# Kernel optimization log

Hardware: AMD Instinct MI355X
Metric: run time of the kernel (lower is better)

Reference implementation:

```python
import jax, jax.numpy as jnp
import numpy as np

DIM = 256
HEADS = 8
H = 56
W = 56
WS = 7          # window size
SHIFT = 3       # cyclic shift
MLP_HIDDEN = 4 * DIM
HEAD_DIM = DIM // HEADS
SCALE = HEAD_DIM ** -0.5
N = WS * WS     # tokens per window
EPS = 1e-5


def _rel_pos_index():
    coords = np.stack(np.meshgrid(np.arange(WS), np.arange(WS), indexing='ij'))  # [2,ws,ws]
    cf = coords.reshape(2, -1)                       # [2, N]
    rel = cf[:, :, None] - cf[:, None, :]            # [2, N, N]
    rel = rel.transpose(1, 2, 0).copy()              # [N, N, 2]
    rel[:, :, 0] += WS - 1
    rel[:, :, 1] += WS - 1
    rel[:, :, 1] *= 2 * WS - 1
    return rel.sum(-1)                               # [N, N]

REL_IDX = jnp.asarray(_rel_pos_index())


def _attn_mask():
    # shifted-window attention mask, computed once (static)
    img = np.zeros((H, W))
    cnt = 0
    slices = (slice(0, -WS), slice(-WS, -SHIFT), slice(-SHIFT, None))
    for hs in slices:
        for ws in slices:
            img[hs, ws] = cnt
            cnt += 1
    mw = img.reshape(H // WS, WS, W // WS, WS).transpose(0, 2, 1, 3).reshape(-1, N)  # [nW, N]
    am = mw[:, None, :] - mw[:, :, None]
    return jnp.asarray(np.where(am != 0, -100.0, 0.0).astype(np.float32))  # [nW, N, N]

ATTN_MASK = _attn_mask()


def _layernorm(y, g, b):
    mu = y.mean(-1, keepdims=True)
    var = ((y - mu) ** 2).mean(-1, keepdims=True)
    return (y - mu) * jax.lax.rsqrt(var + EPS) * g + b


def setup_inputs() -> dict:
    key = jax.random.key(0)
    ks = jax.random.split(key, 10)
    B = 32
    x = jax.random.normal(ks[0], (B, H * W, DIM), dtype=jnp.float32)
    qkv_w = jax.random.normal(ks[1], (DIM, 3 * DIM), dtype=jnp.float32) * 0.02
    qkv_b = jnp.zeros((3 * DIM,), dtype=jnp.float32)
    proj_w = jax.random.normal(ks[2], (DIM, DIM), dtype=jnp.float32) * 0.02
    proj_b = jnp.zeros((DIM,), dtype=jnp.float32)
    bias_table = jax.random.normal(ks[3], ((2 * WS - 1) * (2 * WS - 1), HEADS), dtype=jnp.float32) * 0.02
    norm1_g = jnp.ones((DIM,), dtype=jnp.float32)
    norm1_b = jnp.zeros((DIM,), dtype=jnp.float32)
    norm2_g = jnp.ones((DIM,), dtype=jnp.float32)
    norm2_b = jnp.zeros((DIM,), dtype=jnp.float32)
    mlp_w1 = jax.random.normal(ks[4], (DIM, MLP_HIDDEN), dtype=jnp.float32) * 0.02
    mlp_b1 = jnp.zeros((MLP_HIDDEN,), dtype=jnp.float32)
    mlp_w2 = jax.random.normal(ks[5], (MLP_HIDDEN, DIM), dtype=jnp.float32) * 0.02
    mlp_b2 = jnp.zeros((DIM,), dtype=jnp.float32)
    return dict(x=x, norm1_g=norm1_g, norm1_b=norm1_b, qkv_w=qkv_w, qkv_b=qkv_b,
                proj_w=proj_w, proj_b=proj_b, bias_table=bias_table,
                norm2_g=norm2_g, norm2_b=norm2_b,
                mlp_w1=mlp_w1, mlp_b1=mlp_b1, mlp_w2=mlp_w2, mlp_b2=mlp_b2)


def reference(x, norm1_g, norm1_b, qkv_w, qkv_b, proj_w, proj_b, bias_table,
              norm2_g, norm2_b, mlp_w1, mlp_b1, mlp_w2, mlp_b2):
    B, M, C = x.shape
    shortcut = x
    y = _layernorm(x, norm1_g, norm1_b).reshape(B, H, W, C)
    # cyclic shift
    y = jnp.roll(y, (-SHIFT, -SHIFT), axis=(1, 2))
    # window partition: [B,H,W,C] -> [B*nW, N, C]
    win = y.reshape(B, H // WS, WS, W // WS, WS, C).transpose(0, 1, 3, 2, 4, 5).reshape(-1, N, C)
    Bw = win.shape[0]
    qkv = (win @ qkv_w + qkv_b).reshape(Bw, N, 3, HEADS, HEAD_DIM).transpose(2, 0, 3, 1, 4)
    q, k, v = qkv[0], qkv[1], qkv[2]               # each [Bw, heads, N, hd]
    attn = jnp.einsum('bhnd,bhmd->bhnm', q, k) * SCALE
    bias = bias_table[REL_IDX].transpose(2, 0, 1)  # [heads, N, N]
    attn = attn + bias[None]
    nW = ATTN_MASK.shape[0]
    attn = attn.reshape(B, nW, HEADS, N, N) + ATTN_MASK[None, :, None]
    attn = jax.nn.softmax(attn.reshape(Bw, HEADS, N, N), axis=-1)
    out = jnp.einsum('bhnm,bhmd->bhnd', attn, v).transpose(0, 2, 1, 3).reshape(Bw, N, C)
    out = out @ proj_w + proj_b
    # window reverse and un-shift
    out = out.reshape(B, H // WS, W // WS, WS, WS, C).transpose(0, 1, 3, 2, 4, 5).reshape(B, H, W, C)
    out = jnp.roll(out, (SHIFT, SHIFT), axis=(1, 2)).reshape(B, M, C)
    x = shortcut + out
    h = _layernorm(x, norm2_g, norm2_b)
    h = jax.nn.gelu(h @ mlp_w1 + mlp_b1) @ mlp_w2 + mlp_b2
    return x + h
```

## Files before the change

kernel.cpp:

```cpp
#include <hip/hip_runtime.h>
#include <hip/hip_bf16.h>
#include <math.h>

typedef __bf16 bf16_t;
typedef __attribute__((ext_vector_type(8))) __bf16 bf16x8;
typedef __attribute__((ext_vector_type(4))) __bf16 bf16x4;
typedef __attribute__((ext_vector_type(4))) float f32x4;

#define T_TOK 100352
#define DIMC 256
#define HEADS 8
#define HD 32
#define NTOK 49
#define SHIFT3 3
#define HH 56
#define SCALE_QK 0.17677669529663687f

__device__ __forceinline__ int xrow_of(int rr) {
    int wi = rr / 49; int t = rr - wi * 49;
    int b = wi >> 6; int w64 = wi & 63;
    int wh = w64 >> 3, ww = w64 & 7;
    int i = t / 7, j = t - i * 7;
    int hy = wh * 7 + i, wy = ww * 7 + j;
    int hx = hy + SHIFT3; if (hx >= HH) hx -= HH;
    int wx = wy + SHIFT3; if (wx >= HH) wx -= HH;
    return b * (HH * HH) + hx * HH + wx;
}

__global__ __launch_bounds__(256) void transpose_all(const float* __restrict__ qkv_w,
                                                     const float* __restrict__ proj_w,
                                                     const float* __restrict__ w1,
                                                     const float* __restrict__ w2,
                                                     bf16_t* __restrict__ wt_qkv,
                                                     bf16_t* __restrict__ wt_proj,
                                                     bf16_t* __restrict__ wt_mlp1,
                                                     bf16_t* __restrict__ wt_mlp2) {
    int t = blockIdx.x * 256 + threadIdx.x;
    const float* W; bf16_t* WT; int K, Nc;
    if (t < 196608)      { W = qkv_w;  WT = wt_qkv;  K = 256;  Nc = 768;  }
    else if (t < 262144) { W = proj_w; WT = wt_proj; K = 256;  Nc = 256;  t -= 196608; }
    else if (t < 524288) { W = w1;     WT = wt_mlp1; K = 256;  Nc = 1024; t -= 262144; }
    else                 { W = w2;     WT = wt_mlp2; K = 1024; Nc = 256;  t -= 524288; }
    int k = t / Nc, c = t - k * Nc;
    WT[(size_t)c * K + k] = (bf16_t)W[t];
}

template <int MAP>
__global__ __launch_bounds__(256) void ln_kernel(const float* __restrict__ x,
                                                 const float* __restrict__ g,
                                                 const float* __restrict__ bsh,
                                                 bf16_t* __restrict__ out) {
    int wv = threadIdx.x >> 6, l = threadIdx.x & 63;
    int r = blockIdx.x * 4 + wv;
    int xr = MAP ? xrow_of(r) : r;
    float4 v = ((const float4*)(x + (size_t)xr * DIMC))[l];
    float s = v.x + v.y + v.z + v.w;
    float sq = v.x * v.x + v.y * v.y + v.z * v.z + v.w * v.w;
    #pragma unroll
    for (int off = 32; off; off >>= 1) {
        s += __shfl_down(s, off);
        sq += __shfl_down(sq, off);
    }
    s = __shfl(s, 0); sq = __shfl(sq, 0);
    float mean = s * (1.f / 256.f);
    float var = sq * (1.f / 256.f) - mean * mean;
    float rstd = rsqrtf(var + 1e-5f);
    float4 gv = ((const float4*)g)[l];
    float4 bv = ((const float4*)bsh)[l];
    bf16x4 o;
    o[0] = (bf16_t)((v.x - mean) * rstd * gv.x + bv.x);
    o[1] = (bf16_t)((v.y - mean) * rstd * gv.y + bv.y);
    o[2] = (bf16_t)((v.z - mean) * rstd * gv.z + bv.z);
    o[3] = (bf16_t)((v.w - mean) * rstd * gv.w + bv.w);
    *(bf16x4*)(out + (size_t)r * DIMC + l * 4) = o;
}

template <int EPI, int KT>
__global__ __launch_bounds__(512, 4) void gemm_a(const bf16_t* __restrict__ A,
                                                 const bf16_t* __restrict__ BT,
                                                 const float* __restrict__ bias,
                                                 int Nc,
                                                 bf16_t* __restrict__ outb,
                                                 float* __restrict__ outf,
                                                 const float* __restrict__ resid) {
    constexpr int NS = KT / 32;
    __shared__ __align__(16) char S[3][24576];
    int tid = threadIdx.x;
    int wv = tid >> 6, l = tid & 63;
    int wr = wv >> 2, wc = wv & 3;
    int nTilesN = Nc >> 8;
    int qn = gridDim.x >> 3;
    int lb = (blockIdx.x & 7) * qn + (blockIdx.x >> 3);
    int bm = lb / nTilesN, bn = lb - bm * nTilesN;
    size_t row0 = (size_t)bm * 128;
    int col0 = bn * 256;

    const char* Abase = (const char*)(A + row0 * KT);
    const char* Bbase = (const char*)(BT + (size_t)col0 * KT);
    const size_t ldb = (size_t)KT * 2;

    auto STAGE = [&](int b, int kk) {
        {
            int ci = tid;
            int sup = ci >> 3, slot = ci & 7;
            int us = slot ^ (sup & 7);
            int row = 2 * sup + (us >> 2), ch = us & 3;
            __builtin_amdgcn_global_load_lds(
                (const __attribute__((address_space(1))) void*)(Abase + (size_t)row * ldb + (size_t)kk * 2 + ch * 16),
                (__attribute__((address_space(3))) void*)(S[b] + ci * 16), 16, 0, 0);
        }
        #pragma unroll
        for (int it = 0; it < 2; ++it) {
            int ci = tid + it * 512;
            int sup = ci >> 3, slot = ci & 7;
            int us = slot ^ (sup & 7);
            int row = 2 * sup + (us >> 2), ch = us & 3;
            __builtin_amdgcn_global_load_lds(
                (const __attribute__((address_space(1))) void*)(Bbase + (size_t)row * ldb + (size_t)kk * 2 + ch * 16),
                (__attribute__((address_space(3))) void*)(S[b] + 8192 + ci * 16), 16, 0, 0);
        }
    };

    f32x4 acc[4][4] = {};
    const int lr = l & 15, g4 = l >> 4;

    STAGE(0, 0);
    STAGE(1, 32);

    #pragma unroll
    for (int s = 0; s < NS; ++s) {
        if (s + 1 < NS) { asm volatile("s_waitcnt vmcnt(3)" ::: "memory"); }
        else            { asm volatile("s_waitcnt vmcnt(0)" ::: "memory"); }
        __builtin_amdgcn_s_barrier();
        __builtin_amdgcn_sched_barrier(0);
        int buf = s % 3;
        if (s + 2 < NS) STAGE((s + 2) % 3, (s + 2) * 32);
        const char* Sb = S[buf];
        bf16x8 a[4], b[4];
        #pragma unroll
        for (int mt = 0; mt < 4; ++mt) {
            int r = wr * 64 + mt * 16 + lr;
            int sup = r >> 1;
            int us = ((r & 1) << 2) | g4;
            a[mt] = *(const bf16x8*)(Sb + sup * 128 + ((us ^ (sup & 7)) * 16));
        }
        #pragma unroll
        for (int nt = 0; nt < 4; ++nt) {
            int rc = wc * 64 + nt * 16 + lr;
            int sup = rc >> 1;
            int us = ((rc & 1) << 2) | g4;
            b[nt] = *(const bf16x8*)(Sb + 8192 + sup * 128 + ((us ^ (sup & 7)) * 16));
        }
        __builtin_amdgcn_s_setprio(1);
        #pragma unroll
        for (int mt = 0; mt < 4; ++mt)
            #pragma unroll
            for (int nt = 0; nt < 4; ++nt)
                acc[mt][nt] = __builtin_amdgcn_mfma_f32_16x16x32_bf16(a[mt], b[nt], acc[mt][nt], 0, 0, 0);
        __builtin_amdgcn_s_setprio(0);
        __builtin_amdgcn_sched_barrier(0);
    }

    #pragma unroll
    for (int m = 0; m < 4; ++m) {
        #pragma unroll
        for (int i = 0; i < 4; ++i) {
            int rr = (int)row0 + wr * 64 + m * 16 + g4 * 4 + i;
            size_t orow = (EPI == 3) ? (size_t)xrow_of(rr) * DIMC : (size_t)rr * Nc;
            #pragma unroll
            for (int n = 0; n < 4; ++n) {
                int cc = col0 + wc * 64 + n * 16 + lr;
                float v = acc[m][n][i] + bias[cc];
                if (EPI == 0) {
                    outb[(size_t)rr * Nc + cc] = (bf16_t)v;
                } else if (EPI == 1) {
                    float t3 = v + 0.044715f * v * v * v;
                    float e = __expf(-1.5957691216057308f * t3);
                    float gl = v * __builtin_amdgcn_rcpf(1.f + e);
                    outb[(size_t)rr * Nc + cc] = (bf16_t)gl;
                } else if (EPI == 2) {
                    size_t o = (size_t)rr * Nc + cc;
                    outf[o] = v + resid[o];
                } else {
                    size_t o = orow + cc;
                    outf[o] = v + resid[o];
                }
            }
        }
    }
}

template <int EPI, int KT>
__global__ __launch_bounds__(1024, 4) void gemm_b(const bf16_t* __restrict__ A,
                                                  const bf16_t* __restrict__ BT,
                                                  const float* __restrict__ bias,
                                                  int Nc,
                                                  bf16_t* __restrict__ outb,
                                                  float* __restrict__ outf,
                                                  const float* __restrict__ resid) {
    constexpr int NS = KT / 32;
    __shared__ __align__(16) char S[3][32768];
    int tid = threadIdx.x;
    int wv = tid >> 6, l = tid & 63;
    int wr = wv >> 2, wc = wv & 3;
    int nTilesN = Nc >> 8;
    int qn = gridDim.x >> 3;
    int lb = (blockIdx.x & 7) * qn + (blockIdx.x >> 3);
    int bm = lb / nTilesN, bn = lb - bm * nTilesN;
    size_t row0 = (size_t)bm * 256;
    int col0 = bn * 256;

    const char* Abase = (const char*)(A + row0 * KT);
    const char* Bbase = (const char*)(BT + (size_t)col0 * KT);
    const size_t ldb = (size_t)KT * 2;

    auto STAGE = [&](int b, int kk) {
        int sup = tid >> 3, slot = tid & 7;
        int us = slot ^ (sup & 7);
        int row = 2 * sup + (us >> 2), ch = us & 3;
        __builtin_amdgcn_global_load_lds(
            (const __attribute__((address_space(1))) void*)(Abase + (size_t)row * ldb + (size_t)kk * 2 + ch * 16),
            (__attribute__((address_space(3))) void*)(S[b] + tid * 16), 16, 0, 0);
        __builtin_amdgcn_global_load_lds(
            (const __attribute__((address_space(1))) void*)(Bbase + (size_t)row * ldb + (size_t)kk * 2 + ch * 16),
            (__attribute__((address_space(3))) void*)(S[b] + 16384 + tid * 16), 16, 0, 0);
    };

    f32x4 acc[4][4] = {};
    const int lr = l & 15, g4 = l >> 4;

    STAGE(0, 0);
    STAGE(1, 32);

    #pragma unroll
    for (int s = 0; s < NS; ++s) {
        if (s + 1 < NS) { asm volatile("s_waitcnt vmcnt(2)" ::: "memory"); }
        else            { asm volatile("s_waitcnt vmcnt(0)" ::: "memory"); }
        __builtin_amdgcn_s_barrier();
        __builtin_amdgcn_sched_barrier(0);
        int buf = s % 3;
        if (s + 2 < NS) STAGE((s + 2) % 3, (s + 2) * 32);
        const char* Sb = S[buf];
        bf16x8 a[4], b[4];
        #pragma unroll
        for (int mt = 0; mt < 4; ++mt) {
            int r = wr * 64 + mt * 16 + lr;
            int sup = r >> 1;
            int us = ((r & 1) << 2) | g4;
            a[mt] = *(const bf16x8*)(Sb + sup * 128 + ((us ^ (sup & 7)) * 16));
        }
        #pragma unroll
        for (int nt = 0; nt < 4; ++nt) {
            int rc = wc * 64 + nt * 16 + lr;
            int sup = rc >> 1;
            int us = ((rc & 1) << 2) | g4;
            b[nt] = *(const bf16x8*)(Sb + 16384 + sup * 128 + ((us ^ (sup & 7)) * 16));
        }
        __builtin_amdgcn_s_setprio(1);
        #pragma unroll
        for (int mt = 0; mt < 4; ++mt)
            #pragma unroll
            for (int nt = 0; nt < 4; ++nt)
                acc[mt][nt] = __builtin_amdgcn_mfma_f32_16x16x32_bf16(a[mt], b[nt], acc[mt][nt], 0, 0, 0);
        __builtin_amdgcn_s_setprio(0);
        __builtin_amdgcn_sched_barrier(0);
    }

    #pragma unroll
    for (int m = 0; m < 4; ++m) {
        #pragma unroll
        for (int i = 0; i < 4; ++i) {
            int rr = (int)row0 + wr * 64 + m * 16 + g4 * 4 + i;
            size_t orow = (EPI == 3) ? (size_t)xrow_of(rr) * DIMC : (size_t)rr * Nc;
            #pragma unroll
            for (int n = 0; n < 4; ++n) {
                int cc = col0 + wc * 64 + n * 16 + lr;
                float v = acc[m][n][i] + bias[cc];
                if (EPI == 0) {
                    outb[(size_t)rr * Nc + cc] = (bf16_t)v;
                } else if (EPI == 1) {
                    float t3 = v + 0.044715f * v * v * v;
                    float e = __expf(-1.5957691216057308f * t3);
                    float gl = v * __builtin_amdgcn_rcpf(1.f + e);
                    outb[(size_t)rr * Nc + cc] = (bf16_t)gl;
                } else if (EPI == 2) {
                    size_t o = (size_t)rr * Nc + cc;
                    outf[o] = v + resid[o];
                } else {
                    size_t o = orow + cc;
                    outf[o] = v + resid[o];
                }
            }
        }
    }
}

__global__ __launch_bounds__(256) void attn_mfma(const bf16_t* __restrict__ qkv,
                                                 const float* __restrict__ bt,
                                                 bf16_t* __restrict__ out) {
    __shared__ __align__(16) char lds[4][12800];
    int wv = threadIdx.x >> 6, l = threadIdx.x & 63;
    int head = ((blockIdx.x & 1) << 2) | wv;
    int wi = blockIdx.x >> 1;
    char* W = lds[wv];
    bf16_t* Vt = (bf16_t*)(W + 8192);
    size_t rowbase = (size_t)wi * NTOK;
    const bf16_t* src = qkv + rowbase * 768 + head * HD;

    int w64 = wi & 63;
    int wh = w64 >> 3, ww = w64 & 7;
    bool lastH = (wh == 7), lastW = (ww == 7);
    bool masked = lastH || lastW;

    #pragma unroll
    for (int it = 0; it < 4; ++it) {
        int t = l + it * 64;
        int r = t >> 2, g = t & 3;
        if (r < NTOK) {
            bf16x8 qv = *(const bf16x8*)(src + (size_t)r * 768 + g * 8);
            bf16x8 kv = *(const bf16x8*)(src + (size_t)r * 768 + 256 + g * 8);
            int sa = (r * 64 + g * 16) ^ ((r & 7) << 4);
            *(bf16x8*)(W + sa) = qv;
            *(bf16x8*)(W + 4096 + sa) = kv;
        }
    }
    #pragma unroll
    for (int it = 0; it < 4; ++it) {
        int t = l + it * 64;
        int m = t >> 2, dc = t & 3;
        if (m < NTOK) {
            bf16x8 vv = *(const bf16x8*)(src + (size_t)m * 768 + 512 + dc * 8);
            #pragma unroll
            for (int j = 0; j < 8; ++j) Vt[(dc * 8 + j) * 72 + m] = vv[j];
        } else {
            #pragma unroll
            for (int j = 0; j < 8; ++j) Vt[(dc * 8 + j) * 72 + m] = (bf16_t)0.f;
        }
    }

    int lr = l & 15, g4 = l >> 4;

    bf16x8 a[4], b[4];
    #pragma unroll
    for (int mt = 0; mt < 4; ++mt) {
        int r = mt * 16 + lr;
        int sa = (r * 64 + g4 * 16) ^ ((r & 7) << 4);
        a[mt] = *(const bf16x8*)(W + sa);
        b[mt] = *(const bf16x8*)(W + 4096 + sa);
    }
    f32x4 z = {0.f, 0.f, 0.f, 0.f};
    f32x4 S[4][4];
    #pragma unroll
    for (int mt = 0; mt < 4; ++mt)
        #pragma unroll
        for (int nt = 0; nt < 4; ++nt)
            S[mt][nt] = __builtin_amdgcn_mfma_f32_16x16x32_bf16(a[mt], b[nt], z, 0, 0, 0);

    int i2[4], j2[4], reg2[4];
    #pragma unroll
    for (int nt = 0; nt < 4; ++nt) {
        int cm = nt * 16 + lr;
        i2[nt] = (cm * 147) >> 10;
        j2[nt] = cm - i2[nt] * 7;
        int rh = lastH ? ((i2[nt] < 4) ? 1 : 2) : 0;
        int rw = lastW ? ((j2[nt] < 4) ? 1 : 2) : 0;
        reg2[nt] = rh * 3 + rw;
    }

    #pragma unroll
    for (int mt = 0; mt < 4; ++mt) {
        #pragma unroll
        for (int i = 0; i < 4; ++i) {
            int rn = mt * 16 + g4 * 4 + i;
            bool rowok = rn < NTOK;
            int i1 = (rn * 147) >> 10, j1 = rn - i1 * 7;
            int rh1 = lastH ? ((i1 < 4) ? 1 : 2) : 0;
            int rw1 = lastW ? ((j1 < 4) ? 1 : 2) : 0;
            int reg1 = rh1 * 3 + rw1;
            float sv[4];
            #pragma unroll
            for (int nt = 0; nt < 4; ++nt) {
                int cm = nt * 16 + lr;
                float sc;
                if (rowok && cm < NTOK) {
                    sc = S[mt][nt][i] * SCALE_QK;
                    sc += bt[((i1 - i2[nt] + 6) + 13 * (j1 - j2[nt] + 6)) * 8 + head];
                    if (masked && (reg1 != reg2[nt])) sc -= 100.f;
                } else {
                    sc = -1e30f;
                }
                sv[nt] = sc;
            }
            float mx = fmaxf(fmaxf(sv[0], sv[1]), fmaxf(sv[2], sv[3]));
            mx = fmaxf(mx, __shfl_xor(mx, 1));
            mx = fmaxf(mx, __shfl_xor(mx, 2));
            mx = fmaxf(mx, __shfl_xor(mx, 4));
            mx = fmaxf(mx, __shfl_xor(mx, 8));
            float e[4];
            float sum = 0.f;
            #pragma unroll
            for (int nt = 0; nt < 4; ++nt) { e[nt] = __expf(sv[nt] - mx); sum += e[nt]; }
            sum += __shfl_xor(sum, 1);
            sum += __shfl_xor(sum, 2);
            sum += __shfl_xor(sum, 4);
            sum += __shfl_xor(sum, 8);
            float inv = 1.f / sum;
            #pragma unroll
            for (int nt = 0; nt < 4; ++nt) {
                int cm = nt * 16 + lr;
                int pa = (rn * 128 + cm * 2) ^ ((rn & 7) << 4);
                *(bf16_t*)(W + pa) = (bf16_t)(e[nt] * inv);
            }
        }
    }

    f32x4 o[4][2] = {};
    #pragma unroll
    for (int ks = 0; ks < 2; ++ks) {
        bf16x8 pa[4], vb[2];
        #pragma unroll
        for (int mt = 0; mt < 4; ++mt) {
            int r = mt * 16 + lr;
            int ad = (r * 128 + ks * 64 + g4 * 16) ^ ((r & 7) << 4);
            pa[mt] = *(const bf16x8*)(W + ad);
        }
        #pragma unroll
        for (int dt = 0; dt < 2; ++dt) {
            int d = dt * 16 + lr;
            vb[dt] = *(const bf16x8*)((char*)Vt + d * 144 + ks * 64 + g4 * 16);
        }
        #pragma unroll
        for (int mt = 0; mt < 4; ++mt)
            #pragma unroll
            for (int dt = 0; dt < 2; ++dt)
                o[mt][dt] = __builtin_amdgcn_mfma_f32_16x16x32_bf16(pa[mt], vb[dt], o[mt][dt], 0, 0, 0);
    }

    #pragma unroll
    for (int mt = 0; mt < 4; ++mt) {
        #pragma unroll
        for (int i = 0; i < 4; ++i) {
            int n = mt * 16 + g4 * 4 + i;
            if (n < NTOK) {
                #pragma unroll
                for (int dt = 0; dt < 2; ++dt) {
                    out[(rowbase + n) * DIMC + head * HD + dt * 16 + lr] = (bf16_t)o[mt][dt][i];
                }
            }
        }
    }
}

extern "C" void kernel_launch(void* const* d_in, const int* in_sizes, int n_in,
                              void* d_out, int out_size, void* d_ws, size_t ws_size,
                              hipStream_t stream) {
    const float* x      = (const float*)d_in[0];
    const float* n1g    = (const float*)d_in[1];
    const float* n1b    = (const float*)d_in[2];
    const float* qkv_w  = (const float*)d_in[3];
    const float* qkv_b  = (const float*)d_in[4];
    const float* proj_w = (const float*)d_in[5];
    const float* proj_b = (const float*)d_in[6];
    const float* btab   = (const float*)d_in[7];
    const float* n2g    = (const float*)d_in[8];
    const float* n2b    = (const float*)d_in[9];
    const float* w1     = (const float*)d_in[10];
    const float* b1     = (const float*)d_in[11];
    const float* w2     = (const float*)d_in[12];
    const float* b2     = (const float*)d_in[13];

    char* ws = (char*)d_ws;
    bf16_t* win      = (bf16_t*)(ws);
    bf16_t* qkvbuf   = (bf16_t*)(ws + (size_t)T_TOK * 256 * 2);
    bf16_t* mlp1_buf = (bf16_t*)(ws);
    bf16_t* h2       = (bf16_t*)(ws + (size_t)T_TOK * 2048);
    char* wtp        = ws + (size_t)T_TOK * 2048 + (size_t)T_TOK * 512;
    bf16_t* wt_qkv   = (bf16_t*)wtp;
    bf16_t* wt_proj  = wt_qkv + 768 * 256;
    bf16_t* wt_mlp1  = wt_proj + 256 * 256;
    bf16_t* wt_mlp2  = wt_mlp1 + 1024 * 256;
    float* xmid      = (float*)d_out;

    transpose_all<<<3072, 256, 0, stream>>>(qkv_w, proj_w, w1, w2,
                                            wt_qkv, wt_proj, wt_mlp1, wt_mlp2);

    ln_kernel<1><<<T_TOK / 4, 256, 0, stream>>>(x, n1g, n1b, win);
    gemm_a<0, 256><<<(T_TOK / 128) * (768 / 256), 512, 0, stream>>>(win, wt_qkv, qkv_b, 768,
                                                                    qkvbuf, nullptr, nullptr);
    attn_mfma<<<2048 * 2, 256, 0, stream>>>(qkvbuf, btab, win);
    gemm_a<3, 256><<<(T_TOK / 128) * (256 / 256), 512, 0, stream>>>(win, wt_proj, proj_b, 256,
                                                                    nullptr, xmid, x);
    ln_kernel<0><<<T_TOK / 4, 256, 0, stream>>>(xmid, n2g, n2b, h2);
    gemm_a<1, 256><<<(T_TOK / 128) * (1024 / 256), 512, 0, stream>>>(h2, wt_mlp1, b1, 1024,
                                                                     mlp1_buf, nullptr, nullptr);
    gemm_b<2, 1024><<<(T_TOK / 256) * (256 / 256), 1024, 0, stream>>>(mlp1_buf, wt_mlp2, b2, 256,
                                                                      nullptr, xmid, xmid);
}
```

Measured before the change: 498.9 us.

## Double-buffer MLP2 GEMM with 64-wide K tiles and load attention Q/K directly

The MLP2 GEMM moves from a triple-buffered 32-wide K tile to a double-buffered 64-wide K tile in a 128 KB LDS buffer. It uses a row-XOR swizzle and adds a second barrier before refilling the buffer just consumed, which halves the outer iterations but leaves less prefetch depth. The attention kernel also stops staging Q and K through LDS and loads the MFMA operand fragments straight from global memory, removing LDS writes and reads. The direct loads read padded rows past the 49 real tokens, which belong to the next window or, for the last window, lie past the end of the buffer.

Result: no change. 497.7 us (median of 2 runs) (-0.2%).

```diff
diff --git a/kernel.cpp b/kernel.cpp
--- a/kernel.cpp
+++ b/kernel.cpp
@@ -191,15 +191,15 @@
 }
 
 template <int EPI, int KT>
-__global__ __launch_bounds__(1024, 4) void gemm_b(const bf16_t* __restrict__ A,
-                                                  const bf16_t* __restrict__ BT,
-                                                  const float* __restrict__ bias,
-                                                  int Nc,
-                                                  bf16_t* __restrict__ outb,
-                                                  float* __restrict__ outf,
-                                                  const float* __restrict__ resid) {
-    constexpr int NS = KT / 32;
-    __shared__ __align__(16) char S[3][32768];
+__global__ __launch_bounds__(1024, 4) void gemm_b2(const bf16_t* __restrict__ A,
+                                                   const bf16_t* __restrict__ BT,
+                                                   const float* __restrict__ bias,
+                                                   int Nc,
+                                                   bf16_t* __restrict__ outb,
+                                                   float* __restrict__ outf,
+                                                   const float* __restrict__ resid) {
+    constexpr int NS = KT / 64;
+    __shared__ __align__(16) char S[2][65536];
     int tid = threadIdx.x;
     int wv = tid >> 6, l = tid & 63;
     int wr = wv >> 2, wc = wv & 3;
@@ -215,55 +215,59 @@
     const size_t ldb = (size_t)KT * 2;
 
     auto STAGE = [&](int b, int kk) {
-        int sup = tid >> 3, slot = tid & 7;
-        int us = slot ^ (sup & 7);
-        int row = 2 * sup + (us >> 2), ch = us & 3;
-        __builtin_amdgcn_global_load_lds(
-            (const __attribute__((address_space(1))) void*)(Abase + (size_t)row * ldb + (size_t)kk * 2 + ch * 16),
-            (__attribute__((address_space(3))) void*)(S[b] + tid * 16), 16, 0, 0);
-        __builtin_amdgcn_global_load_lds(
-            (const __attribute__((address_space(1))) void*)(Bbase + (size_t)row * ldb + (size_t)kk * 2 + ch * 16),
-            (__attribute__((address_space(3))) void*)(S[b] + 16384 + tid * 16), 16, 0, 0);
+        #pragma unroll
+        for (int it = 0; it < 2; ++it) {
+            int ci = tid + it * 1024;
+            int row = ci >> 3, ch = ci & 7;
+            int sc = ch ^ (row & 7);
+            __builtin_amdgcn_global_load_lds(
+                (const __attribute__((address_space(1))) void*)(Abase + (size_t)row * ldb + (size_t)kk * 2 + sc * 16),
+                (__attribute__((address_space(3))) void*)(S[b] + ci * 16), 16, 0, 0);
+            __builtin_amdgcn_global_load_lds(
+                (const __attribute__((address_space(1))) void*)(Bbase + (size_t)row * ldb + (size_t)kk * 2 + sc * 16),
+                (__attribute__((address_space(3))) void*)(S[b] + 32768 + ci * 16), 16, 0, 0);
+        }
     };
 
     f32x4 acc[4][4] = {};
     const int lr = l & 15, g4 = l >> 4;
 
     STAGE(0, 0);
-    STAGE(1, 32);
+    STAGE(1, 64);
 
     #pragma unroll
     for (int s = 0; s < NS; ++s) {
-        if (s + 1 < NS) { asm volatile("s_waitcnt vmcnt(2)" ::: "memory"); }
+        if (s + 1 < NS) { asm volatile("s_waitcnt vmcnt(4)" ::: "memory"); }
         else            { asm volatile("s_waitcnt vmcnt(0)" ::: "memory"); }
         __builtin_amdgcn_s_barrier();
         __builtin_amdgcn_sched_barrier(0);
-        int buf = s % 3;
-        if (s + 2 < NS) STAGE((s + 2) % 3, (s + 2) * 32);
-        const char* Sb = S[buf];
-        bf16x8 a[4], b[4];
-        #pragma unroll
-        for (int mt = 0; mt < 4; ++mt) {
-            int r = wr * 64 + mt * 16 + lr;
-            int sup = r >> 1;
-            int us = ((r & 1) << 2) | g4;
-            a[mt] = *(const bf16x8*)(Sb + sup * 128 + ((us ^ (sup & 7)) * 16));
-        }
-        #pragma unroll
-        for (int nt = 0; nt < 4; ++nt) {
-            int rc = wc * 64 + nt * 16 + lr;
-            int sup = rc >> 1;
-            int us = ((rc & 1) << 2) | g4;
-            b[nt] = *(const bf16x8*)(Sb + 16384 + sup * 128 + ((us ^ (sup & 7)) * 16));
-        }
-        __builtin_amdgcn_s_setprio(1);
-        #pragma unroll
-        for (int mt = 0; mt < 4; ++mt)
-            #pragma unroll
-            for (int nt = 0; nt < 4; ++nt)
-                acc[mt][nt] = __builtin_amdgcn_mfma_f32_16x16x32_bf16(a[mt], b[nt], acc[mt][nt], 0, 0, 0);
-        __builtin_amdgcn_s_setprio(0);
+        int buf = s & 1;
+        #pragma unroll
+        for (int ks = 0; ks < 2; ++ks) {
+            bf16x8 a[4], b[4];
+            #pragma unroll
+            for (int mt = 0; mt < 4; ++mt) {
+                int r = wr * 64 + mt * 16 + lr;
+                int c = (ks * 4 + g4) ^ (r & 7);
+                a[mt] = *(const bf16x8*)(S[buf] + r * 128 + c * 16);
+            }
+            #pragma unroll
+            for (int nt = 0; nt < 4; ++nt) {
+                int rc = wc * 64 + nt * 16 + lr;
+                int c = (ks * 4 + g4) ^ (rc & 7);
+                b[nt] = *(const bf16x8*)(S[buf] + 32768 + rc * 128 + c * 16);
+            }
+            __builtin_amdgcn_s_setprio(1);
+            #pragma unroll
+            for (int mt = 0; mt < 4; ++mt)
+                #pragma unroll
+                for (int nt = 0; nt < 4; ++nt)
+                    acc[mt][nt] = __builtin_amdgcn_mfma_f32_16x16x32_bf16(a[mt], b[nt], acc[mt][nt], 0, 0, 0);
+            __builtin_amdgcn_s_setprio(0);
+        }
+        __builtin_amdgcn_s_barrier();
         __builtin_amdgcn_sched_barrier(0);
+        if (s + 2 < NS) STAGE(buf, (s + 2) * 64);
     }
 
     #pragma unroll
@@ -271,7 +275,6 @@
         #pragma unroll
         for (int i = 0; i < 4; ++i) {
             int rr = (int)row0 + wr * 64 + m * 16 + g4 * 4 + i;
-            size_t orow = (EPI == 3) ? (size_t)xrow_of(rr) * DIMC : (size_t)rr * Nc;
             #pragma unroll
             for (int n = 0; n < 4; ++n) {
                 int cc = col0 + wc * 64 + n * 16 + lr;
@@ -283,11 +286,8 @@
                     float e = __expf(-1.5957691216057308f * t3);
                     float gl = v * __builtin_amdgcn_rcpf(1.f + e);
                     outb[(size_t)rr * Nc + cc] = (bf16_t)gl;
-                } else if (EPI == 2) {
+                } else {
                     size_t o = (size_t)rr * Nc + cc;
-                    outf[o] = v + resid[o];
-                } else {
-                    size_t o = orow + cc;
                     outf[o] = v + resid[o];
                 }
             }
@@ -315,18 +315,6 @@
     #pragma unroll
     for (int it = 0; it < 4; ++it) {
         int t = l + it * 64;
-        int r = t >> 2, g = t & 3;
-        if (r < NTOK) {
-            bf16x8 qv = *(const bf16x8*)(src + (size_t)r * 768 + g * 8);
-            bf16x8 kv = *(const bf16x8*)(src + (size_t)r * 768 + 256 + g * 8);
-            int sa = (r * 64 + g * 16) ^ ((r & 7) << 4);
-            *(bf16x8*)(W + sa) = qv;
-            *(bf16x8*)(W + 4096 + sa) = kv;
-        }
-    }
-    #pragma unroll
-    for (int it = 0; it < 4; ++it) {
-        int t = l + it * 64;
         int m = t >> 2, dc = t & 3;
         if (m < NTOK) {
             bf16x8 vv = *(const bf16x8*)(src + (size_t)m * 768 + 512 + dc * 8);
@@ -344,9 +332,8 @@
     #pragma unroll
     for (int mt = 0; mt < 4; ++mt) {
         int r = mt * 16 + lr;
-        int sa = (r * 64 + g4 * 16) ^ ((r & 7) << 4);
-        a[mt] = *(const bf16x8*)(W + sa);
-        b[mt] = *(const bf16x8*)(W + 4096 + sa);
+        a[mt] = *(const bf16x8*)(src + (size_t)r * 768 + g4 * 8);
+        b[mt] = *(const bf16x8*)(src + (size_t)r * 768 + 256 + g4 * 8);
     }
     f32x4 z = {0.f, 0.f, 0.f, 0.f};
     f32x4 S[4][4];
@@ -493,6 +480,6 @@
     ln_kernel<0><<<T_TOK / 4, 256, 0, stream>>>(xmid, n2g, n2b, h2);
     gemm_a<1, 256><<<(T_TOK / 128) * (1024 / 256), 512, 0, stream>>>(h2, wt_mlp1, b1, 1024,
                                                                      mlp1_buf, nullptr, nullptr);
-    gemm_b<2, 1024><<<(T_TOK / 256) * (256 / 256), 1024, 0, stream>>>(mlp1_buf, wt_mlp2, b2, 256,
-                                                                      nullptr, xmid, xmid);
-}
+    gemm_b2<2, 1024><<<(T_TOK / 256) * (256 / 256), 1024, 0, stream>>>(mlp1_buf, wt_mlp2, b2, 256,
+                                                                       nullptr, xmid, xmid);
+}
```

## Switch GEMMs to double-buffered LDS and load attention Q/K fragments from global

Applied to the files above, without the earlier changes.

Both GEMM kernels drop from three to two LDS stage buffers. The next prefetch is now issued after the MFMA block, behind an extra barrier, so the freed buffer is reused safely. This cuts LDS per block, which may allow more resident blocks, at the cost of an extra barrier per k-step and less prefetch distance. The attention kernel loads Q and K MFMA fragments straight from global memory instead of staging them through swizzled LDS. Padding rows 49-63 now read into neighbouring windows, or past the end of the buffer for the last window. The unused EPI==3 scatter path is also removed from gemm_b.

Measured after the change: 516.8 us. 1.04x slower.

```diff
diff --git a/kernel.cpp b/kernel.cpp
--- a/kernel.cpp
+++ b/kernel.cpp
@@ -84,7 +84,7 @@
                                                  float* __restrict__ outf,
                                                  const float* __restrict__ resid) {
     constexpr int NS = KT / 32;
-    __shared__ __align__(16) char S[3][24576];
+    __shared__ __align__(16) char S[2][24576];
     int tid = threadIdx.x;
     int wv = tid >> 6, l = tid & 63;
     int wr = wv >> 2, wc = wv & 3;
@@ -125,7 +125,7 @@
     const int lr = l & 15, g4 = l >> 4;
 
     STAGE(0, 0);
-    STAGE(1, 32);
+    if (NS > 1) STAGE(1, 32);
 
     #pragma unroll
     for (int s = 0; s < NS; ++s) {
@@ -133,8 +133,7 @@
         else            { asm volatile("s_waitcnt vmcnt(0)" ::: "memory"); }
         __builtin_amdgcn_s_barrier();
         __builtin_amdgcn_sched_barrier(0);
-        int buf = s % 3;
-        if (s + 2 < NS) STAGE((s + 2) % 3, (s + 2) * 32);
+        int buf = s & 1;
         const char* Sb = S[buf];
         bf16x8 a[4], b[4];
         #pragma unroll
@@ -159,6 +158,9 @@
                 acc[mt][nt] = __builtin_amdgcn_mfma_f32_16x16x32_bf16(a[mt], b[nt], acc[mt][nt], 0, 0, 0);
         __builtin_amdgcn_s_setprio(0);
         __builtin_amdgcn_sched_barrier(0);
+        __builtin_amdgcn_s_barrier();
+        __builtin_amdgcn_sched_barrier(0);
+        if (s + 2 < NS) STAGE(buf, (s + 2) * 32);
     }
 
     #pragma unroll
@@ -199,7 +201,7 @@
                                                   float* __restrict__ outf,
                                                   const float* __restrict__ resid) {
     constexpr int NS = KT / 32;
-    __shared__ __align__(16) char S[3][32768];
+    __shared__ __align__(16) char S[2][32768];
     int tid = threadIdx.x;
     int wv = tid >> 6, l = tid & 63;
     int wr = wv >> 2, wc = wv & 3;
@@ -238,8 +240,7 @@
         else            { asm volatile("s_waitcnt vmcnt(0)" ::: "memory"); }
         __builtin_amdgcn_s_barrier();
         __builtin_amdgcn_sched_barrier(0);
-        int buf = s % 3;
-        if (s + 2 < NS) STAGE((s + 2) % 3, (s + 2) * 32);
+        int buf = s & 1;
         const char* Sb = S[buf];
         bf16x8 a[4], b[4];
         #pragma unroll
@@ -264,6 +265,9 @@
                 acc[mt][nt] = __builtin_amdgcn_mfma_f32_16x16x32_bf16(a[mt], b[nt], acc[mt][nt], 0, 0, 0);
         __builtin_amdgcn_s_setprio(0);
         __builtin_amdgcn_sched_barrier(0);
+        __builtin_amdgcn_s_barrier();
+        __builtin_amdgcn_sched_barrier(0);
+        if (s + 2 < NS) STAGE(buf, (s + 2) * 32);
     }
 
     #pragma unroll
@@ -271,7 +275,6 @@
         #pragma unroll
         for (int i = 0; i < 4; ++i) {
             int rr = (int)row0 + wr * 64 + m * 16 + g4 * 4 + i;
-            size_t orow = (EPI == 3) ? (size_t)xrow_of(rr) * DIMC : (size_t)rr * Nc;
             #pragma unroll
             for (int n = 0; n < 4; ++n) {
                 int cc = col0 + wc * 64 + n * 16 + lr;
@@ -283,11 +286,8 @@
                     float e = __expf(-1.5957691216057308f * t3);
                     float gl = v * __builtin_amdgcn_rcpf(1.f + e);
                     outb[(size_t)rr * Nc + cc] = (bf16_t)gl;
-                } else if (EPI == 2) {
+                } else {
                     size_t o = (size_t)rr * Nc + cc;
-                    outf[o] = v + resid[o];
-                } else {
-                    size_t o = orow + cc;
                     outf[o] = v + resid[o];
                 }
             }
@@ -315,18 +315,6 @@
     #pragma unroll
     for (int it = 0; it < 4; ++it) {
         int t = l + it * 64;
-        int r = t >> 2, g = t & 3;
-        if (r < NTOK) {
-            bf16x8 qv = *(const bf16x8*)(src + (size_t)r * 768 + g * 8);
-            bf16x8 kv = *(const bf16x8*)(src + (size_t)r * 768 + 256 + g * 8);
-            int sa = (r * 64 + g * 16) ^ ((r & 7) << 4);
-            *(bf16x8*)(W + sa) = qv;
-            *(bf16x8*)(W + 4096 + sa) = kv;
-        }
-    }
-    #pragma unroll
-    for (int it = 0; it < 4; ++it) {
-        int t = l + it * 64;
         int m = t >> 2, dc = t & 3;
         if (m < NTOK) {
             bf16x8 vv = *(const bf16x8*)(src + (size_t)m * 768 + 512 + dc * 8);
@@ -344,9 +332,8 @@
     #pragma unroll
     for (int mt = 0; mt < 4; ++mt) {
         int r = mt * 16 + lr;
-        int sa = (r * 64 + g4 * 16) ^ ((r & 7) << 4);
-        a[mt] = *(const bf16x8*)(W + sa);
-        b[mt] = *(const bf16x8*)(W + 4096 + sa);
+        a[mt] = *(const bf16x8*)(src + (size_t)r * 768 + g4 * 8);
+        b[mt] = *(const bf16x8*)(src + (size_t)r * 768 + 256 + g4 * 8);
     }
     f32x4 z = {0.f, 0.f, 0.f, 0.f};
     f32x4 S[4][4];
```
